# Kernel optimization log

Measured on AMD Instinct MI355X. Metric: run time of the kernel, lower is better.

## Reference

```python
import jax, jax.numpy as jnp
import numpy as np

B, T, D, H, FF = 4, 2048, 768, 12, 4
DH = D // H


def _ln(x, g, b, eps=1e-5):
    mu = x.mean(-1, keepdims=True)
    var = ((x - mu) ** 2).mean(-1, keepdims=True)
    return (x - mu) * jax.lax.rsqrt(var + eps) * g + b


def setup_inputs() -> dict:
    key = jax.random.key(0)
    ks = jax.random.split(key, 16)
    s = 0.02
    d = {
        'x': jax.random.normal(ks[0], (B, T, D), jnp.float32),
        'Wq': jax.random.normal(ks[1], (D, D), jnp.float32) * s,
        'bq': jnp.zeros((D,), jnp.float32),
        'Wk': jax.random.normal(ks[2], (D, D), jnp.float32) * s,
        'bk': jnp.zeros((D,), jnp.float32),
        'Wv': jax.random.normal(ks[3], (D, D), jnp.float32) * s,
        'bv': jnp.zeros((D,), jnp.float32),
        'Wo': jax.random.normal(ks[4], (D, D), jnp.float32) * s,
        'bo': jnp.zeros((D,), jnp.float32),
        'W1': jax.random.normal(ks[5], (D, D * FF), jnp.float32) * s,
        'b1': jnp.zeros((D * FF,), jnp.float32),
        'W2': jax.random.normal(ks[6], (D * FF, D), jnp.float32) * s,
        'b2': jnp.zeros((D,), jnp.float32),
        'g1': jnp.ones((D,), jnp.float32),
        'be1': jnp.zeros((D,), jnp.float32),
        'g2': jnp.ones((D,), jnp.float32),
        'be2': jnp.zeros((D,), jnp.float32),
        'radius': 64,
    }
    return d


def reference(x, Wq, bq, Wk, bk, Wv, bv, Wo, bo, W1, b1, W2, b2, g1, be1, g2, be2, radius):
    Bc, Tc, Dc = x.shape
    # local mask: blocked (True) where |i-j| > radius (clamping in torch code is a no-op)
    i = jnp.arange(Tc)
    mask = jnp.abs(i[:, None] - i[None, :]) > radius  # [T,T] True = masked

    h = _ln(x, g1, be1)
    q = (h @ Wq + bq).reshape(Bc, Tc, H, DH)
    k = (h @ Wk + bk).reshape(Bc, Tc, H, DH)
    v = (h @ Wv + bv).reshape(Bc, Tc, H, DH)
    scale = 1.0 / jnp.sqrt(jnp.asarray(DH, x.dtype))
    scores = jnp.einsum('bthd,bshd->bhts', q, k) * scale  # [B,H,T,T]
    scores = jnp.where(mask[None, None], -jnp.inf, scores)
    attn = jax.nn.softmax(scores, axis=-1)
    ctx = jnp.einsum('bhts,bshd->bthd', attn, v).reshape(Bc, Tc, Dc)
    x = x + (ctx @ Wo + bo)

    h2 = _ln(x, g2, be2)
    ff = jax.nn.gelu(h2 @ W1 + b1, approximate=False) @ W2 + b2
    return x + ff
```

## Files before the change

kernel.cpp:

```cpp
#include <hip/hip_runtime.h>
#include <hip/hip_bf16.h>

#define B_  4
#define T_  2048
#define D_  768
#define H_  12
#define DH_ 64
#define FF_ 3072

typedef __attribute__((ext_vector_type(8))) short bf16x8;
typedef __attribute__((ext_vector_type(4))) float f32x4;
typedef __attribute__((ext_vector_type(4))) unsigned short us4;

#define MFMA16(a, b, c) __builtin_amdgcn_mfma_f32_16x16x32_bf16((a), (b), (c), 0, 0, 0)

__device__ __forceinline__ unsigned short f2bf(float f) {
    union { float f; unsigned u; } v; v.f = f;
    unsigned r = v.u + 0x7fffu + ((v.u >> 16) & 1u);
    return (unsigned short)(r >> 16);
}
__device__ __forceinline__ float bf2f(unsigned short s) {
    union { unsigned u; float f; } v; v.u = ((unsigned)s) << 16;
    return v.f;
}

__device__ __forceinline__ void gload_lds16(const unsigned short* gp, unsigned short* lp) {
    __builtin_amdgcn_global_load_lds(
        (const __attribute__((address_space(1))) unsigned int*)gp,
        (__attribute__((address_space(3))) unsigned int*)lp,
        16, 0, 0);
}

__global__ __launch_bounds__(256) void tcvt_kernel(
    const float* __restrict__ src, unsigned short* __restrict__ dst, int K, int N)
{
    __shared__ float tile[32][33];
    const int bx = blockIdx.x * 32;
    const int by = blockIdx.y * 32;
    const int tx = threadIdx.x, ty = threadIdx.y;
#pragma unroll
    for (int i = 0; i < 32; i += 8)
        tile[ty + i][tx] = src[(size_t)(by + ty + i) * N + bx + tx];
    __syncthreads();
#pragma unroll
    for (int i = 0; i < 32; i += 8)
        dst[(size_t)(bx + ty + i) * K + by + tx] = f2bf(tile[tx][ty + i]);
}

__global__ __launch_bounds__(256) void tcvt4_kernel(
    const float* __restrict__ s0, const float* __restrict__ s1,
    const float* __restrict__ s2, const float* __restrict__ s3,
    unsigned short* __restrict__ dst)
{
    __shared__ float tile[32][33];
    const int z = blockIdx.z;
    const float* src = (z == 0) ? s0 : (z == 1) ? s1 : (z == 2) ? s2 : s3;
    unsigned short* d = dst + (size_t)z * 589824;
    const int bx = blockIdx.x * 32;
    const int by = blockIdx.y * 32;
    const int tx = threadIdx.x, ty = threadIdx.y;
#pragma unroll
    for (int i = 0; i < 32; i += 8)
        tile[ty + i][tx] = src[(size_t)(by + ty + i) * 768 + bx + tx];
    __syncthreads();
#pragma unroll
    for (int i = 0; i < 32; i += 8)
        d[(size_t)(bx + ty + i) * 768 + by + tx] = f2bf(tile[tx][ty + i]);
}

__global__ __launch_bounds__(256) void ln_kernel(
    const float* __restrict__ x, const float* __restrict__ g,
    const float* __restrict__ be, unsigned short* __restrict__ out)
{
    const int row = blockIdx.x;
    const int t = threadIdx.x;
    const float* xr = x + (size_t)row * D_;
    float v0 = xr[t], v1 = xr[t + 256], v2 = xr[t + 512];
    float s = v0 + v1 + v2;
    float s2 = v0 * v0 + v1 * v1 + v2 * v2;
#pragma unroll
    for (int o = 1; o < 64; o <<= 1) {
        s  += __shfl_xor(s,  o);
        s2 += __shfl_xor(s2, o);
    }
    __shared__ float rs[4], rq[4];
    const int wave = t >> 6;
    if ((t & 63) == 0) { rs[wave] = s; rq[wave] = s2; }
    __syncthreads();
    s  = rs[0] + rs[1] + rs[2] + rs[3];
    s2 = rq[0] + rq[1] + rq[2] + rq[3];
    const float mu = s * (1.0f / D_);
    const float var = s2 * (1.0f / D_) - mu * mu;
    const float rstd = rsqrtf(var + 1e-5f);
    unsigned short* orow = out + (size_t)row * D_;
    orow[t]       = f2bf((v0 - mu) * rstd * g[t]       + be[t]);
    orow[t + 256] = f2bf((v1 - mu) * rstd * g[t + 256] + be[t + 256]);
    orow[t + 512] = f2bf((v2 - mu) * rstd * g[t + 512] + be[t + 512]);
}

__global__ __launch_bounds__(256) void reduce_ln_kernel(
    const unsigned short* __restrict__ p0, const unsigned short* __restrict__ p1,
    const float* __restrict__ x, const float* __restrict__ bo,
    const float* __restrict__ g, const float* __restrict__ be,
    float* __restrict__ x2, unsigned short* __restrict__ h2)
{
    const int row = blockIdx.x;
    const int t = threadIdx.x;
    const size_t base = (size_t)row * D_;
    float v[3];
    float s = 0.0f, s2 = 0.0f;
#pragma unroll
    for (int j = 0; j < 3; ++j) {
        const int c = t + j * 256;
        const float vv = bf2f(p0[base + c]) + bf2f(p1[base + c]) + bo[c] + x[base + c];
        v[j] = vv;
        x2[base + c] = vv;
        s += vv; s2 += vv * vv;
    }
#pragma unroll
    for (int o = 1; o < 64; o <<= 1) {
        s  += __shfl_xor(s,  o);
        s2 += __shfl_xor(s2, o);
    }
    __shared__ float rs[4], rq[4];
    const int wave = t >> 6;
    if ((t & 63) == 0) { rs[wave] = s; rq[wave] = s2; }
    __syncthreads();
    s  = rs[0] + rs[1] + rs[2] + rs[3];
    s2 = rq[0] + rq[1] + rq[2] + rq[3];
    const float mu = s * (1.0f / D_);
    const float var = s2 * (1.0f / D_) - mu * mu;
    const float rstd = rsqrtf(var + 1e-5f);
#pragma unroll
    for (int j = 0; j < 3; ++j) {
        const int c = t + j * 256;
        h2[base + c] = f2bf((v[j] - mu) * rstd * g[c] + be[c]);
    }
}

__global__ __launch_bounds__(256) void reduce_out_kernel(
    const unsigned short* __restrict__ p0, const unsigned short* __restrict__ p1,
    const float* __restrict__ x2, const float* __restrict__ b2,
    float* __restrict__ out)
{
    const int n4 = B_ * T_ * D_ / 4;
    for (int i = blockIdx.x * 256 + threadIdx.x; i < n4; i += gridDim.x * 256) {
        const us4 a = ((const us4*)p0)[i];
        const us4 b = ((const us4*)p1)[i];
        const float4 xr = ((const float4*)x2)[i];
        const int col = (i * 4) % D_;
        float4 o;
        o.x = bf2f(a[0]) + bf2f(b[0]) + b2[col]     + xr.x;
        o.y = bf2f(a[1]) + bf2f(b[1]) + b2[col + 1] + xr.y;
        o.z = bf2f(a[2]) + bf2f(b[2]) + b2[col + 2] + xr.z;
        o.w = bf2f(a[3]) + bf2f(b[3]) + b2[col + 3] + xr.w;
        ((float4*)out)[i] = o;
    }
}

template<int MODE>
__global__ __launch_bounds__(512) void gemm512(
    const unsigned short* __restrict__ A,
    const unsigned short* __restrict__ Bt,
    const float* __restrict__ bias,
    const float* __restrict__ bias2,
    const float* __restrict__ bias3,
    void* __restrict__ outp,
    void* __restrict__ out2,
    void* __restrict__ out3,
    int N, int K, int kLen, int nTilesN, int nTilesMN, long partStride)
{
    __shared__ __align__(16) unsigned short As[128 * 64];
    __shared__ __align__(16) unsigned short Bs[128 * 64];

    const int nwg = gridDim.x;
    const int q = nwg >> 3, rr = nwg & 7;
    const int xcd = blockIdx.x & 7, loc = blockIdx.x >> 3;
    const int swz = (xcd < rr ? xcd * (q + 1) : rr * (q + 1) + (xcd - rr) * q) + loc;
    const int ks  = swz / nTilesMN;
    const int rem = swz - ks * nTilesMN;
    const int m0 = (rem / nTilesN) * 128;
    const int n0 = (rem % nTilesN) * 128;
    const int kOff = ks * kLen;

    const int tid = threadIdx.x;
    const int wv = tid >> 6;
    const int lane = tid & 63;
    const int wr = wv >> 1;
    const int wc = wv & 1;

    f32x4 zero4 = {0.0f, 0.0f, 0.0f, 0.0f};
    f32x4 acc[2][4];
#pragma unroll
    for (int i = 0; i < 2; ++i)
#pragma unroll
        for (int j = 0; j < 4; ++j) acc[i][j] = zero4;

    const int lrow = lane >> 3;
    const int scb = (lane & 7) ^ lrow;
    const size_t ag0 = (size_t)(m0 + wv * 16 + lrow) * K + kOff + scb * 8;
    const size_t ag1 = ag0 + (size_t)8 * K;
    const size_t bg0 = (size_t)(n0 + wv * 16 + lrow) * K + kOff + scb * 8;
    const size_t bg1 = bg0 + (size_t)8 * K;
    unsigned short* AsW = As + wv * 1024;
    unsigned short* BsW = Bs + wv * 1024;

    const int fr = lane & 15;
    const int fg = lane >> 4;
    const int sw = fr & 7;

    const int nk = kLen >> 6;
    for (int kt = 0; kt < nk; ++kt) {
        const int k0 = kt << 6;
        __syncthreads();
        gload_lds16(A  + ag0 + k0, AsW);
        gload_lds16(A  + ag1 + k0, AsW + 512);
        gload_lds16(Bt + bg0 + k0, BsW);
        gload_lds16(Bt + bg1 + k0, BsW + 512);
        __syncthreads();
#pragma unroll
        for (int kk = 0; kk < 2; ++kk) {
            bf16x8 afr[2], bfr[4];
#pragma unroll
            for (int mm = 0; mm < 2; ++mm) {
                const int row = wr * 32 + mm * 16 + fr;
                afr[mm] = *(const bf16x8*)(As + row * 64 + (((kk * 4 + fg) ^ sw) << 3));
            }
#pragma unroll
            for (int nn = 0; nn < 4; ++nn) {
                const int row = wc * 64 + nn * 16 + fr;
                bfr[nn] = *(const bf16x8*)(Bs + row * 64 + (((kk * 4 + fg) ^ sw) << 3));
            }
#pragma unroll
            for (int mm = 0; mm < 2; ++mm)
#pragma unroll
                for (int nn = 0; nn < 4; ++nn)
                    acc[mm][nn] = MFMA16(afr[mm], bfr[nn], acc[mm][nn]);
        }
    }

    const int lc = lane & 15;
    const int lr = (lane >> 4) * 4;
#pragma unroll
    for (int mm = 0; mm < 2; ++mm) {
        const int gm0 = m0 + wr * 32 + mm * 16 + lr;
#pragma unroll
        for (int nn = 0; nn < 4; ++nn) {
            const int gn = n0 + wc * 64 + nn * 16 + lc;
            if (MODE == 4) {
                if (gn < 1536) {
                    const float bv = (gn < 768) ? bias[gn] : bias2[gn - 768];
                    unsigned short* o = (gn < 768) ? (unsigned short*)outp : (unsigned short*)out2;
                    const int col = (gn < 768) ? gn : gn - 768;
#pragma unroll
                    for (int r = 0; r < 4; ++r)
                        o[(size_t)(gm0 + r) * 768 + col] = f2bf(acc[mm][nn][r] + bv);
                } else {
                    const float bv = bias3[gn - 1536];
                    const int b = gm0 / T_;
                    const int tl = gm0 - b * T_;
                    us4 pk;
#pragma unroll
                    for (int r = 0; r < 4; ++r) pk[r] = f2bf(acc[mm][nn][r] + bv);
                    *(us4*)((unsigned short*)out3 + ((size_t)(b * D_ + gn - 1536)) * T_ + tl) = pk;
                }
            } else if (MODE == 5) {
                unsigned short* o = (unsigned short*)outp + (size_t)ks * partStride;
#pragma unroll
                for (int r = 0; r < 4; ++r)
                    o[(size_t)(gm0 + r) * N + gn] = f2bf(acc[mm][nn][r]);
            } else {
                const float bv = bias[gn];
#pragma unroll
                for (int r = 0; r < 4; ++r) {
                    const int gm = gm0 + r;
                    float v = acc[mm][nn][r] + bv;
                    if (MODE == 0) {
                        ((unsigned short*)outp)[(size_t)gm * N + gn] = f2bf(v);
                    } else if (MODE == 2) {
                        v = 0.5f * v * (1.0f + erff(v * 0.70710678118654752f));
                        ((unsigned short*)outp)[(size_t)gm * N + gn] = f2bf(v);
                    }
                }
            }
        }
    }
}

__global__ __launch_bounds__(256) void attn_kernel(
    const unsigned short* __restrict__ Q,
    const unsigned short* __restrict__ Kg,
    const unsigned short* __restrict__ Vt,
    unsigned short* __restrict__ ctx)
{
    __shared__ __align__(16) unsigned short Qs[64][72];
    __shared__ __align__(16) unsigned short KP[192 * 72];
    __shared__ __align__(16) unsigned short Vts[64][200];

    const int tid = threadIdx.x;
    const int lane = tid & 63;
    const int w = tid >> 6;
    const int bid = blockIdx.x;
    const int qt = bid & 31;
    const int h = (bid >> 5) % H_;
    const int b = bid / (32 * H_);
    const int qs = qt * 64;
    const int t0 = qs >= 64 ? qs - 64 : 0;
    const int t1 = (qs + 128 < T_) ? qs + 128 : T_;
    const int KW = t1 - t0;

    for (int s = tid; s < 512; s += 256) {
        const int r = s >> 3, c8 = (s & 7) << 3;
        *(uint4*)&Qs[r][c8] =
            *(const uint4*)&Q[((size_t)(b * T_ + qs + r)) * D_ + h * DH_ + c8];
    }
    unsigned short* Ks = KP;
    for (int s = tid; s < 1536; s += 256) {
        const int r = s >> 3, c8 = (s & 7) << 3;
        uint4 val = {0, 0, 0, 0};
        if (r < KW)
            val = *(const uint4*)&Kg[((size_t)(b * T_ + t0 + r)) * D_ + h * DH_ + c8];
        *(uint4*)&Ks[r * 72 + c8] = val;
    }
    for (int s = tid; s < 1536; s += 256) {
        const int r = s / 24, c8 = (s % 24) << 3;
        uint4 val = {0, 0, 0, 0};
        if (c8 < KW)
            val = *(const uint4*)&Vt[((size_t)((b * H_ + h) * DH_ + r)) * T_ + t0 + c8];
        *(uint4*)&Vts[r][c8] = val;
    }
    __syncthreads();

    f32x4 zero4 = {0.0f, 0.0f, 0.0f, 0.0f};
    f32x4 sa[12];
#pragma unroll
    for (int i = 0; i < 12; ++i) sa[i] = zero4;
#pragma unroll
    for (int ks = 0; ks < 2; ++ks) {
        const bf16x8 aq = *(const bf16x8*)&Qs[w * 16 + (lane & 15)][ks * 32 + (lane >> 4) * 8];
#pragma unroll
        for (int cf = 0; cf < 12; ++cf) {
            const bf16x8 bk = *(const bf16x8*)&Ks[(cf * 16 + (lane & 15)) * 72 + ks * 32 + (lane >> 4) * 8];
            sa[cf] = MFMA16(aq, bk, sa[cf]);
        }
    }
    __syncthreads();

    const int lq = w * 16 + (lane >> 4) * 4;
    float mx[4] = {-1e30f, -1e30f, -1e30f, -1e30f};
#pragma unroll
    for (int cf = 0; cf < 12; ++cf) {
        const int key = t0 + cf * 16 + (lane & 15);
#pragma unroll
        for (int r = 0; r < 4; ++r) {
            const int dd = (qs + lq + r) - key;
            const bool ok = (key < t1) && (dd <= 64) && (dd >= -64);
            const float sv = ok ? sa[cf][r] * 0.125f : -1e30f;
            sa[cf][r] = sv;
            mx[r] = fmaxf(mx[r], sv);
        }
    }
#pragma unroll
    for (int r = 0; r < 4; ++r)
#pragma unroll
        for (int o = 1; o < 16; o <<= 1)
            mx[r] = fmaxf(mx[r], __shfl_xor(mx[r], o));

    unsigned short* Ps = KP;
    float sm[4] = {0.0f, 0.0f, 0.0f, 0.0f};
#pragma unroll
    for (int cf = 0; cf < 12; ++cf) {
#pragma unroll
        for (int r = 0; r < 4; ++r) {
            const float p = __expf(sa[cf][r] - mx[r]);
            sm[r] += p;
            Ps[(lq + r) * 200 + cf * 16 + (lane & 15)] = f2bf(p);
        }
    }
#pragma unroll
    for (int r = 0; r < 4; ++r)
#pragma unroll
        for (int o = 1; o < 16; o <<= 1)
            sm[r] += __shfl_xor(sm[r], o);

    f32x4 oa[4];
#pragma unroll
    for (int i = 0; i < 4; ++i) oa[i] = zero4;
#pragma unroll
    for (int ks = 0; ks < 6; ++ks) {
        const bf16x8 ap = *(const bf16x8*)&Ps[(w * 16 + (lane & 15)) * 200 + ks * 32 + (lane >> 4) * 8];
#pragma unroll
        for (int nf = 0; nf < 4; ++nf) {
            const bf16x8 bv = *(const bf16x8*)&Vts[nf * 16 + (lane & 15)][ks * 32 + (lane >> 4) * 8];
            oa[nf] = MFMA16(ap, bv, oa[nf]);
        }
    }
#pragma unroll
    for (int nf = 0; nf < 4; ++nf) {
#pragma unroll
        for (int r = 0; r < 4; ++r) {
            const float o = oa[nf][r] / sm[r];
            ctx[((size_t)(b * T_ + qs + lq + r)) * D_ + h * DH_ + nf * 16 + (lane & 15)] = f2bf(o);
        }
    }
}

extern "C" void kernel_launch(void* const* d_in, const int* in_sizes, int n_in,
                              void* d_out, int out_size, void* d_ws, size_t ws_size,
                              hipStream_t stream)
{
    const float* x   = (const float*)d_in[0];
    const float* Wq  = (const float*)d_in[1];
    const float* bq  = (const float*)d_in[2];
    const float* Wk  = (const float*)d_in[3];
    const float* bk  = (const float*)d_in[4];
    const float* Wv  = (const float*)d_in[5];
    const float* bv  = (const float*)d_in[6];
    const float* Wo  = (const float*)d_in[7];
    const float* bo  = (const float*)d_in[8];
    const float* W1  = (const float*)d_in[9];
    const float* b1  = (const float*)d_in[10];
    const float* W2  = (const float*)d_in[11];
    const float* b2  = (const float*)d_in[12];
    const float* g1  = (const float*)d_in[13];
    const float* be1 = (const float*)d_in[14];
    const float* g2  = (const float*)d_in[15];
    const float* be2 = (const float*)d_in[16];
    float* out = (float*)d_out;

    unsigned short* wqkv_t = (unsigned short*)d_ws;
    unsigned short* wo_t = wqkv_t + 3 * 589824;
    unsigned short* w1_t = wo_t + 589824;
    unsigned short* w2_t = w1_t + 2359296;
    unsigned short* hbuf = w2_t + 2359296;
    unsigned short* qbuf = hbuf + 6291456;
    float* x2 = (float*)(qbuf + 6291456);
    unsigned short* kbuf = (unsigned short*)(x2 + 6291456);
    unsigned short* vtb  = kbuf + 6291456;
    unsigned short* ffb  = kbuf;

    dim3 tb(32, 8);
    tcvt4_kernel<<<dim3(24, 24, 4), tb, 0, stream>>>(Wq, Wk, Wv, Wo, wqkv_t);
    tcvt_kernel<<<dim3(96, 24), tb, 0, stream>>>(W1, w1_t, 768, 3072);
    tcvt_kernel<<<dim3(24, 96), tb, 0, stream>>>(W2, w2_t, 3072, 768);

    ln_kernel<<<8192, 256, 0, stream>>>(x, g1, be1, hbuf);

    gemm512<4><<<64 * 18, 512, 0, stream>>>(
        hbuf, wqkv_t, bq, bk, bv, qbuf, kbuf, vtb, 2304, 768, 768, 18, 64 * 18, 0);

    attn_kernel<<<1536, 256, 0, stream>>>(qbuf, kbuf, vtb, hbuf);

    gemm512<5><<<64 * 6 * 2, 512, 0, stream>>>(
        hbuf, wo_t, nullptr, nullptr, nullptr, kbuf, nullptr, nullptr,
        768, 768, 384, 6, 64 * 6, 6291456);

    reduce_ln_kernel<<<8192, 256, 0, stream>>>(
        kbuf, kbuf + 6291456, x, bo, g2, be2, x2, qbuf);

    gemm512<2><<<64 * 24, 512, 0, stream>>>(
        qbuf, w1_t, b1, nullptr, nullptr, ffb, nullptr, nullptr,
        3072, 768, 768, 24, 64 * 24, 0);

    gemm512<5><<<64 * 6 * 2, 512, 0, stream>>>(
        ffb, w2_t, nullptr, nullptr, nullptr, hbuf, nullptr, nullptr,
        768, 3072, 1536, 6, 64 * 6, 6291456);

    reduce_out_kernel<<<2048, 256, 0, stream>>>(
        hbuf, hbuf + 6291456, x2, b2, out);
}
```

Measured before the change: 239.5 us.

## Add 256x256-tile triple-buffered GEMM with fused GELU for FFN up-projection

```diff
diff --git a/kernel.cpp b/kernel.cpp
--- a/kernel.cpp
+++ b/kernel.cpp
@@ -282,6 +282,168 @@
                         ((unsigned short*)outp)[(size_t)gm * N + gn] = f2bf(v);
                     }
                 }
+            }
+        }
+    }
+}
+
+__global__ __launch_bounds__(512, 2) void gemm256_gelu(
+    const unsigned short* __restrict__ A,
+    const unsigned short* __restrict__ Bt,
+    const float* __restrict__ bias,
+    unsigned short* __restrict__ outp,
+    int N, int K, int nTilesN)
+{
+    extern __shared__ __align__(16) unsigned short lds[];
+
+    const int nwg = gridDim.x;
+    const int q = nwg >> 3, rr = nwg & 7;
+    const int xcd = blockIdx.x & 7, loc = blockIdx.x >> 3;
+    const int swz = (xcd < rr ? xcd * (q + 1) : rr * (q + 1) + (xcd - rr) * q) + loc;
+    const int m0 = (swz / nTilesN) * 256;
+    const int n0 = (swz % nTilesN) * 256;
+
+    const int tid = threadIdx.x;
+    const int wv = tid >> 6;
+    const int lane = tid & 63;
+    const int wm = wv >> 2;
+    const int wn = wv & 3;
+
+    f32x4 zero4 = {0.0f, 0.0f, 0.0f, 0.0f};
+    f32x4 acc[8][4];
+#pragma unroll
+    for (int i = 0; i < 8; ++i)
+#pragma unroll
+        for (int j = 0; j < 4; ++j) acc[i][j] = zero4;
+
+    const int lrow = lane >> 2;
+    const int scb  = (lane & 3) ^ ((lrow >> 1) & 3);
+    const unsigned short* gA0 = A  + (size_t)(m0 + wv * 16 + lrow) * K + scb * 8;
+    const unsigned short* gA1 = gA0 + (size_t)128 * K;
+    const unsigned short* gB0 = Bt + (size_t)(n0 + wv * 16 + lrow) * K + scb * 8;
+    const unsigned short* gB1 = gB0 + (size_t)128 * K;
+    const int dA0 = wv * 512, dA1 = 4096 + wv * 512;
+    const int dB0 = 8192 + wv * 512, dB1 = 12288 + wv * 512;
+
+    const int fr = lane & 15;
+    const int fg = lane >> 4;
+    const int rb = (fg ^ ((fr >> 1) & 3)) << 3;
+    const int aOff = (wm * 128 + fr) * 32 + rb;
+    const int bOff = 8192 + (wn * 64 + fr) * 32 + rb;
+
+    unsigned short* pc = lds;
+    unsigned short* pn = lds + 16384;
+    unsigned short* ps = lds + 32768;
+
+    const int nk = K >> 5;
+
+    gload_lds16(gA0, pc + dA0); gload_lds16(gA1, pc + dA1);
+    gload_lds16(gB0, pc + dB0); gload_lds16(gB1, pc + dB1);
+    gload_lds16(gA0 + 32, pn + dA0); gload_lds16(gA1 + 32, pn + dA1);
+    gload_lds16(gB0 + 32, pn + dB0); gload_lds16(gB1 + 32, pn + dB1);
+    asm volatile("s_waitcnt vmcnt(4)" ::: "memory");
+    __builtin_amdgcn_s_barrier();
+    asm volatile("" ::: "memory");
+
+    for (int t = 0; t < nk; ++t) {
+        const bool st = (t + 2 < nk);
+        const int kc = (t + 2) << 5;
+
+        bf16x8 b0v = *(const bf16x8*)(pc + bOff);
+        bf16x8 b1v = *(const bf16x8*)(pc + bOff + 512);
+        bf16x8 b2v = *(const bf16x8*)(pc + bOff + 1024);
+        bf16x8 b3v = *(const bf16x8*)(pc + bOff + 1536);
+        bf16x8 a0 = *(const bf16x8*)(pc + aOff);
+        bf16x8 a1 = *(const bf16x8*)(pc + aOff + 512);
+        if (st) gload_lds16(gA0 + kc, ps + dA0);
+        asm volatile("s_waitcnt lgkmcnt(0)" ::: "memory");
+        __builtin_amdgcn_sched_barrier(0);
+        __builtin_amdgcn_s_setprio(1);
+        acc[0][0] = MFMA16(a0, b0v, acc[0][0]);
+        acc[0][1] = MFMA16(a0, b1v, acc[0][1]);
+        acc[0][2] = MFMA16(a0, b2v, acc[0][2]);
+        acc[0][3] = MFMA16(a0, b3v, acc[0][3]);
+        acc[1][0] = MFMA16(a1, b0v, acc[1][0]);
+        acc[1][1] = MFMA16(a1, b1v, acc[1][1]);
+        acc[1][2] = MFMA16(a1, b2v, acc[1][2]);
+        acc[1][3] = MFMA16(a1, b3v, acc[1][3]);
+        __builtin_amdgcn_s_setprio(0);
+        __builtin_amdgcn_s_barrier();
+        asm volatile("" ::: "memory");
+
+        a0 = *(const bf16x8*)(pc + aOff + 1024);
+        a1 = *(const bf16x8*)(pc + aOff + 1536);
+        if (st) gload_lds16(gA1 + kc, ps + dA1);
+        asm volatile("s_waitcnt lgkmcnt(0)" ::: "memory");
+        __builtin_amdgcn_sched_barrier(0);
+        __builtin_amdgcn_s_setprio(1);
+        acc[2][0] = MFMA16(a0, b0v, acc[2][0]);
+        acc[2][1] = MFMA16(a0, b1v, acc[2][1]);
+        acc[2][2] = MFMA16(a0, b2v, acc[2][2]);
+        acc[2][3] = MFMA16(a0, b3v, acc[2][3]);
+        acc[3][0] = MFMA16(a1, b0v, acc[3][0]);
+        acc[3][1] = MFMA16(a1, b1v, acc[3][1]);
+        acc[3][2] = MFMA16(a1, b2v, acc[3][2]);
+        acc[3][3] = MFMA16(a1, b3v, acc[3][3]);
+        __builtin_amdgcn_s_setprio(0);
+        __builtin_amdgcn_s_barrier();
+        asm volatile("" ::: "memory");
+
+        a0 = *(const bf16x8*)(pc + aOff + 2048);
+        a1 = *(const bf16x8*)(pc + aOff + 2560);
+        if (st) gload_lds16(gB0 + kc, ps + dB0);
+        asm volatile("s_waitcnt lgkmcnt(0)" ::: "memory");
+        __builtin_amdgcn_sched_barrier(0);
+        __builtin_amdgcn_s_setprio(1);
+        acc[4][0] = MFMA16(a0, b0v, acc[4][0]);
+        acc[4][1] = MFMA16(a0, b1v, acc[4][1]);
+        acc[4][2] = MFMA16(a0, b2v, acc[4][2]);
+        acc[4][3] = MFMA16(a0, b3v, acc[4][3]);
+        acc[5][0] = MFMA16(a1, b0v, acc[5][0]);
+        acc[5][1] = MFMA16(a1, b1v, acc[5][1]);
+        acc[5][2] = MFMA16(a1, b2v, acc[5][2]);
+        acc[5][3] = MFMA16(a1, b3v, acc[5][3]);
+        __builtin_amdgcn_s_setprio(0);
+        __builtin_amdgcn_s_barrier();
+        asm volatile("" ::: "memory");
+
+        a0 = *(const bf16x8*)(pc + aOff + 3072);
+        a1 = *(const bf16x8*)(pc + aOff + 3584);
+        if (st) gload_lds16(gB1 + kc, ps + dB1);
+        asm volatile("s_waitcnt lgkmcnt(0)" ::: "memory");
+        __builtin_amdgcn_sched_barrier(0);
+        __builtin_amdgcn_s_setprio(1);
+        acc[6][0] = MFMA16(a0, b0v, acc[6][0]);
+        acc[6][1] = MFMA16(a0, b1v, acc[6][1]);
+        acc[6][2] = MFMA16(a0, b2v, acc[6][2]);
+        acc[6][3] = MFMA16(a0, b3v, acc[6][3]);
+        acc[7][0] = MFMA16(a1, b0v, acc[7][0]);
+        acc[7][1] = MFMA16(a1, b1v, acc[7][1]);
+        acc[7][2] = MFMA16(a1, b2v, acc[7][2]);
+        acc[7][3] = MFMA16(a1, b3v, acc[7][3]);
+        __builtin_amdgcn_s_setprio(0);
+        if (st) asm volatile("s_waitcnt vmcnt(4)" ::: "memory");
+        else    asm volatile("s_waitcnt vmcnt(0)" ::: "memory");
+        __builtin_amdgcn_s_barrier();
+        asm volatile("" ::: "memory");
+
+        unsigned short* tmp = pc; pc = pn; pn = ps; ps = tmp;
+    }
+
+    const int lc = lane & 15;
+    const int lr = (lane >> 4) * 4;
+#pragma unroll
+    for (int mm = 0; mm < 8; ++mm) {
+        const int gm0 = m0 + wm * 128 + mm * 16 + lr;
+#pragma unroll
+        for (int nn = 0; nn < 4; ++nn) {
+            const int gn = n0 + wn * 64 + nn * 16 + lc;
+            const float bv = bias[gn];
+#pragma unroll
+            for (int r = 0; r < 4; ++r) {
+                float v = acc[mm][nn][r] + bv;
+                v = 0.5f * v * (1.0f + erff(v * 0.70710678118654752f));
+                outp[(size_t)(gm0 + r) * N + gn] = f2bf(v);
             }
         }
     }
@@ -458,9 +620,8 @@
     reduce_ln_kernel<<<8192, 256, 0, stream>>>(
         kbuf, kbuf + 6291456, x, bo, g2, be2, x2, qbuf);
 
-    gemm512<2><<<64 * 24, 512, 0, stream>>>(
-        qbuf, w1_t, b1, nullptr, nullptr, ffb, nullptr, nullptr,
-        3072, 768, 768, 24, 64 * 24, 0);
+    gemm256_gelu<<<32 * 12, 512, 3 * 32768, stream>>>(
+        qbuf, w1_t, b1, ffb, 3072, 768, 12);
 
     gemm512<5><<<64 * 6 * 2, 512, 0, stream>>>(
         ffb, w2_t, nullptr, nullptr, nullptr, hbuf, nullptr, nullptr,
```

After: 263.4 us. 10.0% more time.
